# Kernel optimization log

Hardware: AMD Instinct MI355X
Metric: run time of the kernel (lower is better)

## Reference

```python
import math
import jax, jax.numpy as jnp
import numpy as np

EPS = 1e-5
B, S, D = 2, 2048, 2048
Z, HD, H, N = 512, 4096, 8, 8
ZH, VH = Z // H, HD // H  # 64, 512
GROUPS = 32


def timestep_norm(x, w, b):
    # cumulative (over time) group normalization; groups of dg channels
    dg = D // GROUPS
    xg = x.reshape(B, S, GROUPS, dg)
    s1 = jnp.cumsum(xg.sum(-1), axis=1)                 # [B,S,G]
    s2 = jnp.cumsum(jnp.square(xg).sum(-1), axis=1)     # [B,S,G]
    cnt = (jnp.arange(S, dtype=x.dtype) + 1.0) * dg
    mean = s1 / cnt[None, :, None]
    var = s2 / cnt[None, :, None] - jnp.square(mean)
    xn = (xg - mean[..., None]) * jax.lax.rsqrt(var[..., None] + EPS)
    return xn.reshape(B, S, D) * w + b


def cema(x, alpha, delta, theta, gamma, omega):
    # complex multi-head EMA: h_t = a*e^{i\theta} x_t + (1-a*d)*e^{i\theta} h_{t-1};
    # y_t = Re(gamma^H h_t) + omega * x_t    (real-arithmetic form, scan over time)
    p = jax.nn.sigmoid(alpha)                      # [D,N]
    qm = 1.0 - p * jax.nn.sigmoid(delta)           # [D,N]
    phase = jax.nn.sigmoid(theta)[:, None] * (2.0 * math.pi * (jnp.arange(N, dtype=x.dtype) + 1.0) / N)
    c, s = jnp.cos(phase), jnp.sin(phase)
    ur, ui = p * c, p * s
    qr, qi = qm * c, qm * s
    gr, gi = gamma[..., 0], gamma[..., 1]

    def step(h, xt):  # xt: [B,D]
        hr, hi = h
        nhr = qr * hr - qi * hi + ur * xt[..., None]
        nhi = qi * hr + qr * hi + ui * xt[..., None]
        y = jnp.sum(nhr * gr + nhi * gi, axis=-1)  # [B,D]
        return (nhr, nhi), y

    h0 = (jnp.zeros((B, D, N), x.dtype), jnp.zeros((B, D, N), x.dtype))
    _, ys = jax.lax.scan(step, h0, jnp.moveaxis(x, 1, 0))
    return jnp.moveaxis(ys, 0, 1) + x * omega


def rmsnorm(x, w=None):
    y = x * jax.lax.rsqrt(jnp.mean(jnp.square(x), axis=-1, keepdims=True) + EPS)
    return y if w is None else y * w


def apply_rotary(xq, xk, freqs):
    # xq/xk: [B,S,H,ZH]; freqs: [S, ZH//2, 2] (cos, sin)
    cos = freqs[None, :, None, :, 0]
    sin = freqs[None, :, None, :, 1]

    def rot(x):
        xr = x.reshape(*x.shape[:-1], ZH // 2, 2)
        re, im = xr[..., 0], xr[..., 1]
        out = jnp.stack([re * cos - im * sin, re * sin + im * cos], axis=-1)
        return out.reshape(x.shape)

    return rot(xq), rot(xk)


def setup_inputs():
    key = jax.random.key(0)
    ks = jax.random.split(key, 24)
    p = 0.02
    inp = {
        "x": jax.random.normal(ks[0], (B, S, D), jnp.float32),
        "tn_weight": 1.0 + p * jax.random.normal(ks[1], (D,), jnp.float32),
        "tn_bias": p * jax.random.normal(ks[2], (D,), jnp.float32),
        "ema_alpha": jax.random.normal(ks[3], (D, N), jnp.float32),
        "ema_delta": jax.random.normal(ks[4], (D, N), jnp.float32),
        "ema_theta": jax.random.normal(ks[5], (D,), jnp.float32),
        "ema_gamma": jax.random.normal(ks[6], (D, N, 2), jnp.float32) / math.sqrt(N),
        "ema_omega": p * jax.random.normal(ks[7], (D,), jnp.float32),
        "rms_weight": 1.0 + p * jax.random.normal(ks[8], (D,), jnp.float32),
        "wz_w": jax.random.normal(ks[9], (D, Z), jnp.float32) / math.sqrt(D),
        "wz_b": p * jax.random.normal(ks[10], (Z,), jnp.float32),
        "wv_w": jax.random.normal(ks[11], (D, HD), jnp.float32) / math.sqrt(D),
        "wv_b": p * jax.random.normal(ks[12], (HD,), jnp.float32),
        "wr_w": jax.random.normal(ks[13], (D, HD), jnp.float32) / math.sqrt(D),
        "wr_b": p * jax.random.normal(ks[14], (HD,), jnp.float32),
        "wh1_w": jax.random.normal(ks[15], (D, D), jnp.float32) / math.sqrt(D),
        "wh1_b": p * jax.random.normal(ks[16], (D,), jnp.float32),
        "wh2_w": jax.random.normal(ks[17], (HD, D), jnp.float32) / math.sqrt(HD),
        "attn_gamma": p * jax.random.normal(ks[18], (2, Z), jnp.float32),
        "attn_beta": p * jax.random.normal(ks[19], (2, Z), jnp.float32),
    }
    # rotary freqs (cos, sin) for head dim ZH
    inv = 1.0 / (10000.0 ** (np.arange(0, ZH, 2, dtype=np.float32) / ZH))
    ang = np.arange(S, dtype=np.float32)[:, None] * inv[None, :]
    inp["freqs_cis"] = jnp.asarray(np.stack([np.cos(ang), np.sin(ang)], axis=-1))
    return inp


def reference(x, freqs_cis, tn_weight, tn_bias, ema_alpha, ema_delta, ema_theta,
              ema_gamma, ema_omega, rms_weight, wz_w, wz_b, wv_w, wv_b, wr_w, wr_b,
              wh1_w, wh1_b, wh2_w, attn_gamma, attn_beta):
    residual = x
    out_tsn = timestep_norm(x, tn_weight, tn_bias)
    out_cema = cema(out_tsn, ema_alpha, ema_delta, ema_theta, ema_gamma, ema_omega)
    mx = rmsnorm(out_cema, rms_weight)

    z = mx @ wz_w + wz_b                              # [B,S,Z]
    z = rmsnorm(z.reshape(B, S, H, ZH)).reshape(B, S, Z)
    gamma = (attn_gamma + 1.0) / math.sqrt(ZH)        # [2,Z]
    z2 = z[:, :, None, :] * gamma + attn_beta         # [B,S,2,Z]
    q, k = z2[:, :, 0], z2[:, :, 1]

    v = jax.nn.silu(out_tsn @ wv_w + wv_b)            # [B,S,HD]
    r = jax.nn.silu(mx @ wr_w + wr_b)                 # [B,S,HD]

    qh = q.reshape(B, S, H, ZH)
    kh = k.reshape(B, S, H, ZH)
    vh = v.reshape(B, S, H, VH)
    qh, kh = apply_rotary(qh, kh, freqs_cis)

    # causal additive mask; scale 1.0 (folded into gamma)
    neg = jnp.finfo(jnp.float32).min
    mask = jnp.where(jnp.tril(jnp.ones((S, S), bool)), 0.0, neg).astype(jnp.float32)
    scores = jnp.einsum('bqhd,bkhd->bhqk', qh, kh) + mask
    probs = jax.nn.softmax(scores.astype(jnp.float32), axis=-1).astype(qh.dtype)
    attn = jnp.einsum('bhqk,bkhd->bqhd', probs, vh).reshape(B, S, HD)

    attn = attn * r
    h = (mx @ wh1_w + wh1_b) + attn @ wh2_w
    return h + residual
```

## Files before the change

### kernel.cpp

```cpp
#include <hip/hip_runtime.h>
#include <stdint.h>


typedef __bf16 bf16_t;
typedef bf16_t bf16x8 __attribute__((ext_vector_type(8)));
typedef float floatx4 __attribute__((ext_vector_type(4)));
typedef __attribute__((address_space(1))) unsigned int as1_uint;
typedef __attribute__((address_space(3))) unsigned int as3_uint;

static constexpr int kB = 2, kS = 2048, kD = 2048;
static constexpr int kZ = 512, kHD = 4096, kH = 8;
static constexpr int kG = 32;
static constexpr int kC = 64, kL = 32;

__device__ __forceinline__ void async16(void* lds, const void* g) {
  __builtin_amdgcn_global_load_lds((const as1_uint*)(size_t)g, (as3_uint*)lds, 16, 0, 0);
}

__device__ __forceinline__ float sigm(float x) { return 1.0f / (1.0f + expf(-x)); }

__global__ __launch_bounds__(256) void wtrans_all(
    const float* __restrict__ wz_w, const float* __restrict__ wv_w,
    const float* __restrict__ wr_w, const float* __restrict__ wh1_w,
    const float* __restrict__ wh2_w, bf16_t* __restrict__ wzT,
    bf16_t* __restrict__ wvT, bf16_t* __restrict__ wrT,
    bf16_t* __restrict__ whcT) {
  __shared__ float tile[32][33];
  const int bid = blockIdx.x;
  const float* W; bf16_t* Wt; int N, ldWt, colOff, nb, sub;
  if (bid < 1024)       { sub = bid;         W = wz_w;  Wt = wzT;  N = kZ;  ldWt = kD;   colOff = 0;    nb = 16;  }
  else if (bid < 9216)  { sub = bid - 1024;  W = wv_w;  Wt = wvT;  N = kHD; ldWt = kD;   colOff = 0;    nb = 128; }
  else if (bid < 17408) { sub = bid - 9216;  W = wr_w;  Wt = wrT;  N = kHD; ldWt = kD;   colOff = 0;    nb = 128; }
  else if (bid < 21504) { sub = bid - 17408; W = wh1_w; Wt = whcT; N = kD;  ldWt = 6144; colOff = 0;    nb = 64;  }
  else                  { sub = bid - 21504; W = wh2_w; Wt = whcT; N = kD;  ldWt = 6144; colOff = 2048; nb = 64;  }
  const int n0 = (sub % nb) * 32, k0 = (sub / nb) * 32;
  const int tx = threadIdx.x & 31, ty = threadIdx.x >> 5;
#pragma unroll
  for (int i = 0; i < 32; i += 8)
    tile[ty + i][tx] = W[(size_t)(k0 + ty + i) * N + n0 + tx];
  __syncthreads();
#pragma unroll
  for (int i = 0; i < 32; i += 8)
    Wt[(size_t)(n0 + ty + i) * ldWt + colOff + k0 + tx] = (bf16_t)tile[tx][ty + i];
}

__global__ __launch_bounds__(256) void tsn_sums(const float* __restrict__ x,
                                                float* __restrict__ g1,
                                                float* __restrict__ g2) {
  int bs = blockIdx.x, t = threadIdx.x;
  const float4* rp = (const float4*)(x + (size_t)bs * kD + t * 8);
  float4 a = rp[0], b = rp[1];
  float s1 = a.x + a.y + a.z + a.w + b.x + b.y + b.z + b.w;
  float s2 = a.x * a.x + a.y * a.y + a.z * a.z + a.w * a.w +
             b.x * b.x + b.y * b.y + b.z * b.z + b.w * b.w;
  s1 += __shfl_xor(s1, 1); s2 += __shfl_xor(s2, 1);
  s1 += __shfl_xor(s1, 2); s2 += __shfl_xor(s2, 2);
  s1 += __shfl_xor(s1, 4); s2 += __shfl_xor(s2, 4);
  if ((t & 7) == 0) {
    int g = t >> 3, b_ = bs >> 11, s = bs & 2047;
    size_t idx = ((size_t)b_ * kG + g) * kS + s;
    g1[idx] = s1; g2[idx] = s2;
  }
}

__global__ __launch_bounds__(256) void tsn_scan(float* __restrict__ g1,
                                                float* __restrict__ g2) {
  __shared__ float wt1[4], wt2[4];
  const int t = threadIdx.x, lane = t & 63, wv = t >> 6;
  size_t base = (size_t)blockIdx.x * kS + t * 8;
  float4 p0 = ((const float4*)(g1 + base))[0];
  float4 p1 = ((const float4*)(g1 + base))[1];
  float4 q0 = ((const float4*)(g2 + base))[0];
  float4 q1 = ((const float4*)(g2 + base))[1];
  float v1[8] = {p0.x, p0.y, p0.z, p0.w, p1.x, p1.y, p1.z, p1.w};
  float v2[8] = {q0.x, q0.y, q0.z, q0.w, q1.x, q1.y, q1.z, q1.w};
  float a1[8], a2[8], s1 = 0.f, s2 = 0.f;
#pragma unroll
  for (int i = 0; i < 8; ++i) {
    s1 += v1[i]; a1[i] = s1;
    s2 += v2[i]; a2[i] = s2;
  }
  float w1 = s1, w2 = s2;
#pragma unroll
  for (int off = 1; off < 64; off <<= 1) {
    float t1 = __shfl_up(w1, off), t2 = __shfl_up(w2, off);
    if (lane >= off) { w1 += t1; w2 += t2; }
  }
  if (lane == 63) { wt1[wv] = w1; wt2[wv] = w2; }
  __syncthreads();
  float add1 = w1 - s1, add2 = w2 - s2;
#pragma unroll
  for (int j = 0; j < 4; ++j)
    if (j < wv) { add1 += wt1[j]; add2 += wt2[j]; }
#pragma unroll
  for (int i = 0; i < 8; ++i) { a1[i] += add1; a2[i] += add2; }
  ((float4*)(g1 + base))[0] = make_float4(a1[0], a1[1], a1[2], a1[3]);
  ((float4*)(g1 + base))[1] = make_float4(a1[4], a1[5], a1[6], a1[7]);
  ((float4*)(g2 + base))[0] = make_float4(a2[0], a2[1], a2[2], a2[3]);
  ((float4*)(g2 + base))[1] = make_float4(a2[4], a2[5], a2[6], a2[7]);
}

__global__ __launch_bounds__(256) void tsn_norm(const float* __restrict__ x,
    const float* __restrict__ g1, const float* __restrict__ g2,
    const float* __restrict__ w, const float* __restrict__ bias,
    float* __restrict__ tsn, bf16_t* __restrict__ tsnb) {
  int bs = blockIdx.x, t = threadIdx.x;
  int b = bs >> 11, s = bs & 2047, g = t >> 3;
  float cnt = (float)(s + 1) * 64.0f;
  size_t gidx = ((size_t)b * kG + g) * kS + s;
  float mean = g1[gidx] / cnt;
  float inv = rsqrtf(g2[gidx] / cnt - mean * mean + 1e-5f);
  size_t base = (size_t)bs * kD + t * 8;
  float4 a = ((const float4*)(x + base))[0];
  float4 c = ((const float4*)(x + base))[1];
  float v[8] = {a.x, a.y, a.z, a.w, c.x, c.y, c.z, c.w};
  float4 w0 = ((const float4*)(w + t * 8))[0], w1 = ((const float4*)(w + t * 8))[1];
  float4 b0 = ((const float4*)(bias + t * 8))[0], b1 = ((const float4*)(bias + t * 8))[1];
  float wv[8] = {w0.x, w0.y, w0.z, w0.w, w1.x, w1.y, w1.z, w1.w};
  float bv[8] = {b0.x, b0.y, b0.z, b0.w, b1.x, b1.y, b1.z, b1.w};
  float r[8];
  bf16x8 ob;
#pragma unroll
  for (int i = 0; i < 8; ++i) {
    r[i] = (v[i] - mean) * inv * wv[i] + bv[i];
    ob[i] = (bf16_t)r[i];
  }
  ((float4*)(tsn + base))[0] = make_float4(r[0], r[1], r[2], r[3]);
  ((float4*)(tsn + base))[1] = make_float4(r[4], r[5], r[6], r[7]);
  *(bf16x8*)(tsnb + base) = ob;
}

__device__ __forceinline__ void cema_coeffs(const float* __restrict__ alpha,
    const float* __restrict__ delta, float st, int d,
    float (&qr)[8], float (&qi)[8], float (&ur)[8], float (&ui)[8]) {
  const float4* ap = (const float4*)(alpha + (size_t)d * 8);
  const float4* dp = (const float4*)(delta + (size_t)d * 8);
  float4 a0 = ap[0], a1 = ap[1], d0 = dp[0], d1 = dp[1];
  float av[8] = {a0.x, a0.y, a0.z, a0.w, a1.x, a1.y, a1.z, a1.w};
  float dv[8] = {d0.x, d0.y, d0.z, d0.w, d1.x, d1.y, d1.z, d1.w};
#pragma unroll
  for (int n = 0; n < 8; ++n) {
    float p = sigm(av[n]);
    float qm = 1.0f - p * sigm(dv[n]);
    float ph = st * (0.78539816339744831f * (float)(n + 1));
    float cs = cosf(ph), sn = sinf(ph);
    qr[n] = qm * cs; qi[n] = qm * sn;
    ur[n] = p * cs;  ui[n] = p * sn;
  }
}

__global__ __launch_bounds__(256) void cema_pass1(const float* __restrict__ tsn,
    const float* __restrict__ alpha, const float* __restrict__ delta,
    const float* __restrict__ theta, float2* __restrict__ hend) {
  int b = blockIdx.x >> 6, c = blockIdx.x & 63;
  int d = blockIdx.y * 256 + threadIdx.x;
  float st = sigm(theta[d]);
  float qr[8], qi[8], ur[8], ui[8];
  cema_coeffs(alpha, delta, st, d, qr, qi, ur, ui);
  float hr[8] = {0}, hi[8] = {0};
  const float* xp = tsn + ((size_t)b * kS + c * kL) * kD + d;
  for (int i = 0; i < kL; ++i) {
    float xt = xp[(size_t)i * kD];
#pragma unroll
    for (int n = 0; n < 8; ++n) {
      float tr = fmaf(qr[n], hr[n], fmaf(-qi[n], hi[n], ur[n] * xt));
      float ti = fmaf(qi[n], hr[n], fmaf(qr[n], hi[n], ui[n] * xt));
      hr[n] = tr; hi[n] = ti;
    }
  }
  float2* op = hend + (((size_t)(b * kC + c)) * kD + d) * 8;
#pragma unroll
  for (int n = 0; n < 8; ++n) op[n] = make_float2(hr[n], hi[n]);
}

__global__ __launch_bounds__(256) void cema_pass2(const float2* __restrict__ hend,
    const float* __restrict__ alpha, const float* __restrict__ delta,
    const float* __restrict__ theta, float2* __restrict__ hinit) {
  int tid = blockIdx.x * 256 + threadIdx.x;
  int n = tid & 7, d = (tid >> 3) & 2047, b = tid >> 14;
  int dn = d * 8 + n;
  float p = sigm(alpha[dn]);
  float qm = 1.0f - p * sigm(delta[dn]);
  float ph = sigm(theta[d]) * (0.78539816339744831f * (float)(n + 1));
  float ar = qm * cosf(ph), ai = qm * sinf(ph);
#pragma unroll
  for (int t = 0; t < 5; ++t) {
    float nr = ar * ar - ai * ai;
    ai = 2.0f * ar * ai;
    ar = nr;
  }
  float hr = 0.f, hi = 0.f;
  for (int c = 0; c < kC; ++c) {
    size_t idx = (((size_t)(b * kC + c)) * kD + d) * 8 + n;
    hinit[idx] = make_float2(hr, hi);
    float2 e = hend[idx];
    float nr = fmaf(ar, hr, fmaf(-ai, hi, e.x));
    float ni = fmaf(ai, hr, fmaf(ar, hi, e.y));
    hr = nr; hi = ni;
  }
}

__global__ __launch_bounds__(256) void cema_pass3(const float* __restrict__ tsn,
    const float* __restrict__ alpha, const float* __restrict__ delta,
    const float* __restrict__ theta, const float* __restrict__ gamma,
    const float* __restrict__ omega, const float2* __restrict__ hinit,
    float* __restrict__ outc) {
  int b = blockIdx.x >> 6, c = blockIdx.x & 63;
  int d = blockIdx.y * 256 + threadIdx.x;
  float st = sigm(theta[d]);
  float qr[8], qi[8], ur[8], ui[8];
  cema_coeffs(alpha, delta, st, d, qr, qi, ur, ui);
  float gr[8], gi[8];
  const float4* gp = (const float4*)(gamma + (size_t)d * 16);
#pragma unroll
  for (int m = 0; m < 4; ++m) {
    float4 g = gp[m];
    gr[m * 2] = g.x; gi[m * 2] = g.y; gr[m * 2 + 1] = g.z; gi[m * 2 + 1] = g.w;
  }
  float om = omega[d];
  float hr[8], hi[8];
  const float2* ip = hinit + (((size_t)(b * kC + c)) * kD + d) * 8;
#pragma unroll
  for (int n = 0; n < 8; ++n) { float2 h = ip[n]; hr[n] = h.x; hi[n] = h.y; }
  const float* xp = tsn + ((size_t)b * kS + c * kL) * kD + d;
  float* op = outc + ((size_t)b * kS + c * kL) * kD + d;
  for (int i = 0; i < kL; ++i) {
    float xt = xp[(size_t)i * kD];
    float y = 0.f;
#pragma unroll
    for (int n = 0; n < 8; ++n) {
      float tr = fmaf(qr[n], hr[n], fmaf(-qi[n], hi[n], ur[n] * xt));
      float ti = fmaf(qi[n], hr[n], fmaf(qr[n], hi[n], ui[n] * xt));
      hr[n] = tr; hi[n] = ti;
      y = fmaf(tr, gr[n], fmaf(ti, gi[n], y));
    }
    op[(size_t)i * kD] = fmaf(xt, om, y);
  }
}

__global__ __launch_bounds__(256) void rms_kernel(const float* __restrict__ in,
                                                  const float* __restrict__ w,
                                                  bf16_t* __restrict__ outb) {
  int bs = blockIdx.x, t = threadIdx.x;
  size_t base = (size_t)bs * kD + t * 8;
  float4 a = ((const float4*)(in + base))[0];
  float4 c = ((const float4*)(in + base))[1];
  float v[8] = {a.x, a.y, a.z, a.w, c.x, c.y, c.z, c.w};
  float ss = 0.f;
#pragma unroll
  for (int i = 0; i < 8; ++i) ss += v[i] * v[i];
#pragma unroll
  for (int off = 1; off < 64; off <<= 1) ss += __shfl_xor(ss, off);
  __shared__ float red[4];
  if ((t & 63) == 0) red[t >> 6] = ss;
  __syncthreads();
  ss = red[0] + red[1] + red[2] + red[3];
  float inv = rsqrtf(ss * (1.0f / 2048.0f) + 1e-5f);
  float4 w0 = ((const float4*)(w + t * 8))[0], w1 = ((const float4*)(w + t * 8))[1];
  float wv[8] = {w0.x, w0.y, w0.z, w0.w, w1.x, w1.y, w1.z, w1.w};
  bf16x8 ob;
#pragma unroll
  for (int i = 0; i < 8; ++i) ob[i] = (bf16_t)(v[i] * inv * wv[i]);
  *(bf16x8*)(outb + base) = ob;
}

__global__ __launch_bounds__(256) void zpost_kernel(const float* __restrict__ z,
    const float* __restrict__ ag, const float* __restrict__ ab,
    const float* __restrict__ freqs, bf16_t* __restrict__ q, bf16_t* __restrict__ k) {
  int bs = blockIdx.x, t = threadIdx.x;
  int b = bs >> 11, s = bs & 2047;
  int h = t >> 5, i = t & 31;
  const float* zr = z + (size_t)bs * kZ + h * 64;
  float re = zr[2 * i], im = zr[2 * i + 1];
  float ss = re * re + im * im;
#pragma unroll
  for (int off = 1; off < 32; off <<= 1) ss += __shfl_xor(ss, off);
  float inv = rsqrtf(ss * (1.0f / 64.0f) + 1e-5f);
  float zne = re * inv, zno = im * inv;
  const float rs = 0.125f;
  int ze = h * 64 + 2 * i, zo = ze + 1;
  float qe = zne * ((ag[ze] + 1.f) * rs) + ab[ze];
  float qo = zno * ((ag[zo] + 1.f) * rs) + ab[zo];
  float ke = zne * ((ag[kZ + ze] + 1.f) * rs) + ab[kZ + ze];
  float ko = zno * ((ag[kZ + zo] + 1.f) * rs) + ab[kZ + zo];
  float cs = freqs[((size_t)s * 32 + i) * 2 + 0];
  float sn = freqs[((size_t)s * 32 + i) * 2 + 1];
  size_t o = (((size_t)b * kH + h) * kS + s) * 64 + 2 * i;
  q[o]     = (bf16_t)(qe * cs - qo * sn);
  q[o + 1] = (bf16_t)(qe * sn + qo * cs);
  k[o]     = (bf16_t)(ke * cs - ko * sn);
  k[o + 1] = (bf16_t)(ke * sn + ko * cs);
}

__global__ __launch_bounds__(256) void gemm_fused3(
    const bf16_t* __restrict__ tsnb, const bf16_t* __restrict__ mx,
    const bf16_t* __restrict__ wvT, const bf16_t* __restrict__ wrT,
    const bf16_t* __restrict__ wzT, const float* __restrict__ wv_b,
    const float* __restrict__ wr_b, const float* __restrict__ wz_b,
    bf16_t* __restrict__ vTb, bf16_t* __restrict__ rb,
    float* __restrict__ zbuf) {
  __shared__ __align__(16) bf16_t sA[2][128 * 32];
  __shared__ __align__(16) bf16_t sB[2][128 * 32];
  const int bid = blockIdx.x;
  const bf16_t* A; const bf16_t* Bt; const float* bias;
  int N, epi, sub;
  if (bid < 1024)      { sub = bid;        A = tsnb; Bt = wvT; bias = wv_b; N = kHD; epi = 1; }
  else if (bid < 2048) { sub = bid - 1024; A = mx;   Bt = wrT; bias = wr_b; N = kHD; epi = 2; }
  else                 { sub = bid - 2048; A = mx;   Bt = wzT; bias = wz_b; N = kZ;  epi = 0; }
  const int m0 = (sub & 31) * 128, n0 = (sub >> 5) * 128;
  const int t = threadIdx.x;
  const int wave = t >> 6, lane = t & 63;
  const int quad = lane >> 4, l16 = lane & 15;
  const int wm = (wave >> 1) * 64, wn = (wave & 1) * 64;
  const int K = kD;

  floatx4 acc[4][4];
#pragma unroll
  for (int i = 0; i < 4; ++i)
#pragma unroll
    for (int j = 0; j < 4; ++j) acc[i][j] = (floatx4){0.f, 0.f, 0.f, 0.f};

  const int seg0 = wave * 64 + lane;
  const int seg1 = 256 + wave * 64 + lane;
  const int r0 = seg0 >> 2, c0 = (seg0 & 3) * 8;
  const int r1 = seg1 >> 2, c1 = (seg1 & 3) * 8;

  auto stage = [&](int buf, int kt) {
    async16(sA[buf] + (size_t)(wave * 64) * 8,       A + (size_t)(m0 + r0) * K + kt + c0);
    async16(sA[buf] + (size_t)(256 + wave * 64) * 8, A + (size_t)(m0 + r1) * K + kt + c1);
    async16(sB[buf] + (size_t)(wave * 64) * 8,       Bt + (size_t)(n0 + r0) * K + kt + c0);
    async16(sB[buf] + (size_t)(256 + wave * 64) * 8, Bt + (size_t)(n0 + r1) * K + kt + c1);
  };

  stage(0, 0);
  __syncthreads();

  const int nsteps = K >> 5;
  for (int st = 0; st < nsteps; ++st) {
    const int cur = st & 1;
    if (st + 1 < nsteps) stage(cur ^ 1, (st + 1) << 5);

    bf16x8 af[4], bfr[4];
#pragma unroll
    for (int i = 0; i < 4; ++i)
      af[i] = *(const bf16x8*)(sA[cur] + (wm + i * 16 + l16) * 32 + quad * 8);
#pragma unroll
    for (int j = 0; j < 4; ++j)
      bfr[j] = *(const bf16x8*)(sB[cur] + (wn + j * 16 + l16) * 32 + quad * 8);
#pragma unroll
    for (int i = 0; i < 4; ++i)
#pragma unroll
      for (int j = 0; j < 4; ++j)
        acc[i][j] = __builtin_amdgcn_mfma_f32_16x16x32_bf16(af[i], bfr[j], acc[i][j], 0, 0, 0);

    __syncthreads();
  }

#pragma unroll
  for (int i = 0; i < 4; ++i) {
#pragma unroll
    for (int j = 0; j < 4; ++j) {
#pragma unroll
      for (int r = 0; r < 4; ++r) {
        int row = m0 + wm + i * 16 + quad * 4 + r;
        int col = n0 + wn + j * 16 + l16;
        size_t idx = (size_t)row * N + col;
        float v = acc[i][j][r];
        if (epi == 0) {
          zbuf[idx] = v + bias[col];
        } else if (epi == 1) {
          v += bias[col];
          v = v / (1.f + __expf(-v));
          size_t vidx = ((size_t)(row >> 11) * kHD + col) * (size_t)kS + (row & 2047);
          vTb[vidx] = (bf16_t)v;
        } else {
          v += bias[col];
          v = v / (1.f + __expf(-v));
          rb[idx] = (bf16_t)v;
        }
      }
    }
  }
}

__global__ __launch_bounds__(256) void gemm_bt(const bf16_t* __restrict__ A1,
    int lda1, const bf16_t* __restrict__ A2, int lda2, int K1,
    const bf16_t* __restrict__ Bt, int M, int N, int K,
    const float* __restrict__ bias, const float* __restrict__ add1,
    float* __restrict__ outF) {
  __shared__ __align__(16) bf16_t sA[2][128 * 32];
  __shared__ __align__(16) bf16_t sB[2][128 * 32];
  const int t = threadIdx.x;
  const int wave = t >> 6, lane = t & 63;
  const int quad = lane >> 4, l16 = lane & 15;
  const int m0 = blockIdx.x * 128, n0 = blockIdx.y * 128;
  const int wm = (wave >> 1) * 64, wn = (wave & 1) * 64;

  floatx4 acc[4][4];
#pragma unroll
  for (int i = 0; i < 4; ++i)
#pragma unroll
    for (int j = 0; j < 4; ++j) acc[i][j] = (floatx4){0.f, 0.f, 0.f, 0.f};

  const int seg0 = wave * 64 + lane;
  const int seg1 = 256 + wave * 64 + lane;
  const int r0 = seg0 >> 2, c0 = (seg0 & 3) * 8;
  const int r1 = seg1 >> 2, c1 = (seg1 & 3) * 8;

  auto stage = [&](int buf, int kt) {
    const bf16_t* Ab; int ldab; int kk;
    if (kt < K1) { Ab = A1; ldab = lda1; kk = kt; }
    else         { Ab = A2; ldab = lda2; kk = kt - K1; }
    async16(sA[buf] + (size_t)(wave * 64) * 8,       Ab + (size_t)(m0 + r0) * ldab + kk + c0);
    async16(sA[buf] + (size_t)(256 + wave * 64) * 8, Ab + (size_t)(m0 + r1) * ldab + kk + c1);
    async16(sB[buf] + (size_t)(wave * 64) * 8,       Bt + (size_t)(n0 + r0) * K + kt + c0);
    async16(sB[buf] + (size_t)(256 + wave * 64) * 8, Bt + (size_t)(n0 + r1) * K + kt + c1);
  };

  stage(0, 0);
  __syncthreads();

  const int nsteps = K >> 5;
  for (int st = 0; st < nsteps; ++st) {
    const int cur = st & 1;
    if (st + 1 < nsteps) stage(cur ^ 1, (st + 1) << 5);

    bf16x8 af[4], bfr[4];
#pragma unroll
    for (int i = 0; i < 4; ++i)
      af[i] = *(const bf16x8*)(sA[cur] + (wm + i * 16 + l16) * 32 + quad * 8);
#pragma unroll
    for (int j = 0; j < 4; ++j)
      bfr[j] = *(const bf16x8*)(sB[cur] + (wn + j * 16 + l16) * 32 + quad * 8);
#pragma unroll
    for (int i = 0; i < 4; ++i)
#pragma unroll
      for (int j = 0; j < 4; ++j)
        acc[i][j] = __builtin_amdgcn_mfma_f32_16x16x32_bf16(af[i], bfr[j], acc[i][j], 0, 0, 0);

    __syncthreads();
  }

#pragma unroll
  for (int i = 0; i < 4; ++i) {
#pragma unroll
    for (int j = 0; j < 4; ++j) {
#pragma unroll
      for (int r = 0; r < 4; ++r) {
        int row = m0 + wm + i * 16 + quad * 4 + r;
        int col = n0 + wn + j * 16 + l16;
        size_t idx = (size_t)row * N + col;
        outF[idx] = acc[i][j][r] + bias[col] + add1[idx];
      }
    }
  }
}

__global__ __launch_bounds__(256) void attn_kernel(const bf16_t* __restrict__ qg,
    const bf16_t* __restrict__ kg, const bf16_t* __restrict__ vT,
    const bf16_t* __restrict__ rg, bf16_t* __restrict__ attnG) {
  const int bid = blockIdx.x;
  const int qt = (kS / 64 - 1) - (bid >> 5);
  const int bh = (bid >> 1) & 15;
  const int vs = bid & 1;
  const int b = bh >> 3, h = bh & 7;
  const int t = threadIdx.x;
  const int w = t >> 6, lane = t & 63;
  const int quad = lane >> 4, l16 = lane & 15;
  const int q0 = qt * 64;

  __shared__ __align__(16) bf16_t sP[2][64 * 64];
  __shared__ __align__(16) bf16_t sK[2][64 * 64];
  __shared__ float sM[64], sL[64], sAl[2][64];
  if (t < 64) { sM[t] = 0.f; sL[t] = 0.f; }

  const bf16_t* qbase = qg + ((size_t)bh * kS + q0) * 64;
  const bf16_t* kbase = kg + (size_t)bh * kS * 64;
  const bf16_t* vbase = vT + ((size_t)bh * 512 + vs * 256 + w * 64) * kS;

  auto stage_k = [&](bf16_t* dstbuf, int k0) {
#pragma unroll
    for (int half = 0; half < 2; ++half) {
      int seg = half * 256 + w * 64 + lane;
      int r = seg >> 3, cc = seg & 7;
      async16(dstbuf + (size_t)(half * 256 + w * 64) * 8,
              kbase + (size_t)(k0 + r) * 64 + (cc ^ (r & 7)) * 8);
    }
  };

  bf16x8 qfrag[2];
#pragma unroll
  for (int ks = 0; ks < 2; ++ks)
    qfrag[ks] = *(const bf16x8*)(qbase + (size_t)(w * 16 + l16) * 64 + ks * 32 + quad * 8);

  floatx4 oacc[4][4];
#pragma unroll
  for (int i = 0; i < 4; ++i)
#pragma unroll
    for (int j = 0; j < 4; ++j) oacc[i][j] = (floatx4){0.f, 0.f, 0.f, 0.f};

  stage_k(sK[0], 0);
  __syncthreads();

  for (int kt = 0; kt <= qt; ++kt) {
    const int k0 = kt * 64;
    const int pb = kt & 1;

    if (kt < qt) stage_k(sK[pb ^ 1], k0 + 64);

    bf16x8 vf[2][4];
#pragma unroll
    for (int ks = 0; ks < 2; ++ks)
#pragma unroll
      for (int nj = 0; nj < 4; ++nj)
        vf[ks][nj] = *(const bf16x8*)(vbase + (size_t)(nj * 16 + l16) * kS + k0 + ks * 32 + quad * 8);

    floatx4 sacc[4];
#pragma unroll
    for (int nt = 0; nt < 4; ++nt) sacc[nt] = (floatx4){0.f, 0.f, 0.f, 0.f};
#pragma unroll
    for (int ks = 0; ks < 2; ++ks)
#pragma unroll
      for (int nt = 0; nt < 4; ++nt) {
        int row = nt * 16 + l16;
        int ch = (ks * 4 + quad) ^ (row & 7);
        bf16x8 kf = *(const bf16x8*)(sK[pb] + row * 64 + ch * 8);
        sacc[nt] = __builtin_amdgcn_mfma_f32_16x16x32_bf16(qfrag[ks], kf, sacc[nt], 0, 0, 0);
      }
    if (kt == qt) {
#pragma unroll
      for (int nt = 0; nt < 4; ++nt)
#pragma unroll
        for (int r = 0; r < 4; ++r) {
          int sk = k0 + nt * 16 + l16;
          int qq = q0 + w * 16 + quad * 4 + r;
          if (sk > qq) sacc[nt][r] = -1e30f;
        }
    }

    float mo[4], mloc[4], lspec[4];
#pragma unroll
    for (int r = 0; r < 4; ++r) {
      mo[r] = sM[w * 16 + quad * 4 + r];
      mloc[r] = fmaxf(fmaxf(sacc[0][r], sacc[1][r]), fmaxf(sacc[2][r], sacc[3][r]));
    }
#pragma unroll
    for (int r = 0; r < 4; ++r) {
      float s = 0.f;
#pragma unroll
      for (int nt = 0; nt < 4; ++nt) {
        float e = __expf(sacc[nt][r] - mo[r]);
        sacc[nt][r] = e;
        s += e;
      }
      lspec[r] = s;
    }
#pragma unroll
    for (int off = 1; off < 16; off <<= 1)
#pragma unroll
      for (int r = 0; r < 4; ++r) {
        mloc[r] = fmaxf(mloc[r], __shfl_xor(mloc[r], off));
        lspec[r] += __shfl_xor(lspec[r], off);
      }
    float mnew[4], al[4];
#pragma unroll
    for (int r = 0; r < 4; ++r) {
      mnew[r] = fmaxf(mo[r], mloc[r]);
      al[r] = __expf(mo[r] - mnew[r]);
    }
    if (l16 == 0) {
#pragma unroll
      for (int r = 0; r < 4; ++r) {
        int row = w * 16 + quad * 4 + r;
        sM[row] = mnew[r];
        sL[row] = al[r] * (sL[row] + lspec[r]);
        sAl[pb][row] = al[r];
      }
    }
#pragma unroll
    for (int nt = 0; nt < 4; ++nt)
#pragma unroll
      for (int r = 0; r < 4; ++r) {
        int row = w * 16 + quad * 4 + r;
        sP[pb][row * 64 + ((nt * 16 + l16) ^ ((row & 7) << 3))] = (bf16_t)(sacc[nt][r] * al[r]);
      }

    __syncthreads();

#pragma unroll
    for (int mi = 0; mi < 4; ++mi)
#pragma unroll
      for (int r = 0; r < 4; ++r) {
        float a = sAl[pb][mi * 16 + quad * 4 + r];
#pragma unroll
        for (int nj = 0; nj < 4; ++nj) oacc[mi][nj][r] *= a;
      }
    __builtin_amdgcn_s_setprio(1);
#pragma unroll
    for (int ks = 0; ks < 2; ++ks) {
      bf16x8 pa[4];
#pragma unroll
      for (int mi = 0; mi < 4; ++mi) {
        int row = mi * 16 + l16;
        pa[mi] = *(const bf16x8*)(sP[pb] + row * 64 + ((ks * 32 + quad * 8) ^ ((row & 7) << 3)));
      }
#pragma unroll
      for (int nj = 0; nj < 4; ++nj)
#pragma unroll
        for (int mi = 0; mi < 4; ++mi)
          oacc[mi][nj] = __builtin_amdgcn_mfma_f32_16x16x32_bf16(pa[mi], vf[ks][nj], oacc[mi][nj], 0, 0, 0);
    }
    __builtin_amdgcn_s_setprio(0);
  }

#pragma unroll
  for (int mi = 0; mi < 4; ++mi)
#pragma unroll
    for (int r = 0; r < 4; ++r) {
      int srow = q0 + mi * 16 + quad * 4 + r;
      float linv = 1.0f / sL[mi * 16 + quad * 4 + r];
#pragma unroll
      for (int nj = 0; nj < 4; ++nj) {
        int hd = h * 512 + vs * 256 + w * 64 + nj * 16 + l16;
        size_t idx = ((size_t)b * kS + srow) * kHD + hd;
        float rv = (float)rg[idx];
        attnG[idx] = (bf16_t)(oacc[mi][nj][r] * linv * rv);
      }
    }
}

extern "C" void kernel_launch(void* const* d_in, const int* in_sizes, int n_in,
                              void* d_out, int out_size, void* d_ws, size_t ws_size,
                              hipStream_t stream) {
  const float* x      = (const float*)d_in[0];
  const float* tnw    = (const float*)d_in[1];
  const float* tnb    = (const float*)d_in[2];
  const float* ealpha = (const float*)d_in[3];
  const float* edelta = (const float*)d_in[4];
  const float* etheta = (const float*)d_in[5];
  const float* egamma = (const float*)d_in[6];
  const float* eomega = (const float*)d_in[7];
  const float* rmsw   = (const float*)d_in[8];
  const float* wz_w   = (const float*)d_in[9];
  const float* wz_b   = (const float*)d_in[10];
  const float* wv_w   = (const float*)d_in[11];
  const float* wv_b   = (const float*)d_in[12];
  const float* wr_w   = (const float*)d_in[13];
  const float* wr_b   = (const float*)d_in[14];
  const float* wh1_w  = (const float*)d_in[15];
  const float* wh1_b  = (const float*)d_in[16];
  const float* wh2_w  = (const float*)d_in[17];
  const float* ag     = (const float*)d_in[18];
  const float* ab     = (const float*)d_in[19];
  const float* freqs  = (const float*)d_in[20];
  float* out = (float*)d_out;

  char* ws = (char*)d_ws;
  size_t off = 0;
  auto alloc = [&](size_t bytes) -> void* {
    void* p = ws + off;
    off += (bytes + 255) & ~(size_t)255;
    return p;
  };
  float*  tsn  = (float*)alloc(8388608ull * 4);
  bf16_t* tsnb = (bf16_t*)alloc(8388608ull * 2);
  float*  g1   = (float*)alloc(131072ull * 4);
  float*  g2   = (float*)alloc(131072ull * 4);
  float*  cema = (float*)alloc(8388608ull * 4);
  bf16_t* mx   = (bf16_t*)alloc(8388608ull * 2);
  bf16_t* wzT  = (bf16_t*)alloc(1048576ull * 2);
  bf16_t* wvT  = (bf16_t*)alloc(8388608ull * 2);
  bf16_t* wrT  = (bf16_t*)alloc(8388608ull * 2);
  bf16_t* whcT = (bf16_t*)alloc(12582912ull * 2);
  float*  zbuf = (float*)alloc(2097152ull * 4);
  bf16_t* qb   = (bf16_t*)alloc(2097152ull * 2);
  bf16_t* kb   = (bf16_t*)alloc(2097152ull * 2);
  bf16_t* rb   = (bf16_t*)alloc(16777216ull * 2);
  bf16_t* aG   = (bf16_t*)alloc(16777216ull * 2);
  bf16_t* vTb  = (bf16_t*)tsn;
  float*  h1   = cema;
  float2* hend  = (float2*)rb;
  float2* hinit = (float2*)aG;
  (void)h1;

  wtrans_all<<<dim3(29696), 256, 0, stream>>>(wz_w, wv_w, wr_w, wh1_w, wh2_w,
                                              wzT, wvT, wrT, whcT);

  tsn_sums<<<kB * kS, 256, 0, stream>>>(x, g1, g2);
  tsn_scan<<<kB * kG, 256, 0, stream>>>(g1, g2);
  tsn_norm<<<kB * kS, 256, 0, stream>>>(x, g1, g2, tnw, tnb, tsn, tsnb);

  cema_pass1<<<dim3(kB * kC, kD / 256), 256, 0, stream>>>(tsn, ealpha, edelta,
                                                          etheta, hend);
  cema_pass2<<<kB * kD * 8 / 256, 256, 0, stream>>>(hend, ealpha, edelta,
                                                    etheta, hinit);
  cema_pass3<<<dim3(kB * kC, kD / 256), 256, 0, stream>>>(tsn, ealpha, edelta,
      etheta, egamma, eomega, hinit, cema);
  rms_kernel<<<kB * kS, 256, 0, stream>>>(cema, rmsw, mx);

  const int M = kB * kS;
  gemm_fused3<<<dim3(2176), 256, 0, stream>>>(tsnb, mx, wvT, wrT, wzT,
      wv_b, wr_b, wz_b, vTb, rb, zbuf);
  zpost_kernel<<<kB * kS, 256, 0, stream>>>(zbuf, ag, ab, freqs, qb, kb);
  attn_kernel<<<dim3(1024), 256, 0, stream>>>(qb, kb, vTb, rb, aG);
  gemm_bt<<<dim3(M / 128, kD / 128), 256, 0, stream>>>(mx, kD, aG, kHD, kD,
      whcT, M, kD, 6144, wh1_b, x, out);
  (void)in_sizes; (void)n_in; (void)out_size; (void)ws_size;
}
```

Baseline: 835.8 us.

## Use 8-wave blocks for final GEMM and XCD-aware attention block mapping

The final output GEMM now runs with 512 threads (8 waves) per 128x128 tile, each wave computing a 64x32 sub-tile, so each thread issues half as many async loads and holds half the accumulators. This aims to raise occupancy and latency hiding for the K=6144 GEMM. The attention kernel's block-index decode is also remapped so that each (batch, head) is pinned to one XCD (bid&7), meant to improve L2 reuse of K/V across query tiles. Risks: smaller per-wave tiles lower MFMA-to-LDS-read ratio and add sync cost.

```diff
diff --git a/kernel.cpp b/kernel.cpp
--- a/kernel.cpp
+++ b/kernel.cpp
@@ -383,38 +383,33 @@
   }
 }
 
-__global__ __launch_bounds__(256) void gemm_bt(const bf16_t* __restrict__ A1,
-    int lda1, const bf16_t* __restrict__ A2, int lda2, int K1,
-    const bf16_t* __restrict__ Bt, int M, int N, int K,
-    const float* __restrict__ bias, const float* __restrict__ add1,
+__global__ __launch_bounds__(512) void gemm_whc8(const bf16_t* __restrict__ mx,
+    const bf16_t* __restrict__ aG, const bf16_t* __restrict__ whcT,
+    const float* __restrict__ wh1_b, const float* __restrict__ x,
     float* __restrict__ outF) {
   __shared__ __align__(16) bf16_t sA[2][128 * 32];
   __shared__ __align__(16) bf16_t sB[2][128 * 32];
   const int t = threadIdx.x;
-  const int wave = t >> 6, lane = t & 63;
+  const int wid = t >> 6, lane = t & 63;
   const int quad = lane >> 4, l16 = lane & 15;
   const int m0 = blockIdx.x * 128, n0 = blockIdx.y * 128;
-  const int wm = (wave >> 1) * 64, wn = (wave & 1) * 64;
-
-  floatx4 acc[4][4];
+  const int wm = (wid >> 2) * 64, wn = (wid & 3) * 32;
+  const int N = kD, K = 6144, K1 = kD;
+
+  floatx4 acc[4][2];
 #pragma unroll
   for (int i = 0; i < 4; ++i)
 #pragma unroll
-    for (int j = 0; j < 4; ++j) acc[i][j] = (floatx4){0.f, 0.f, 0.f, 0.f};
-
-  const int seg0 = wave * 64 + lane;
-  const int seg1 = 256 + wave * 64 + lane;
-  const int r0 = seg0 >> 2, c0 = (seg0 & 3) * 8;
-  const int r1 = seg1 >> 2, c1 = (seg1 & 3) * 8;
+    for (int j = 0; j < 2; ++j) acc[i][j] = (floatx4){0.f, 0.f, 0.f, 0.f};
+
+  const int r0 = t >> 2, c0 = (t & 3) * 8;
 
   auto stage = [&](int buf, int kt) {
     const bf16_t* Ab; int ldab; int kk;
-    if (kt < K1) { Ab = A1; ldab = lda1; kk = kt; }
-    else         { Ab = A2; ldab = lda2; kk = kt - K1; }
-    async16(sA[buf] + (size_t)(wave * 64) * 8,       Ab + (size_t)(m0 + r0) * ldab + kk + c0);
-    async16(sA[buf] + (size_t)(256 + wave * 64) * 8, Ab + (size_t)(m0 + r1) * ldab + kk + c1);
-    async16(sB[buf] + (size_t)(wave * 64) * 8,       Bt + (size_t)(n0 + r0) * K + kt + c0);
-    async16(sB[buf] + (size_t)(256 + wave * 64) * 8, Bt + (size_t)(n0 + r1) * K + kt + c1);
+    if (kt < K1) { Ab = mx; ldab = kD;  kk = kt; }
+    else         { Ab = aG; ldab = kHD; kk = kt - K1; }
+    async16(sA[buf] + (size_t)(wid * 64) * 8, Ab + (size_t)(m0 + r0) * ldab + kk + c0);
+    async16(sB[buf] + (size_t)(wid * 64) * 8, whcT + (size_t)(n0 + r0) * 6144 + kt + c0);
   };
 
   stage(0, 0);
@@ -425,44 +420,43 @@
     const int cur = st & 1;
     if (st + 1 < nsteps) stage(cur ^ 1, (st + 1) << 5);
 
-    bf16x8 af[4], bfr[4];
+    bf16x8 af[4], bfr[2];
 #pragma unroll
     for (int i = 0; i < 4; ++i)
       af[i] = *(const bf16x8*)(sA[cur] + (wm + i * 16 + l16) * 32 + quad * 8);
 #pragma unroll
-    for (int j = 0; j < 4; ++j)
+    for (int j = 0; j < 2; ++j)
       bfr[j] = *(const bf16x8*)(sB[cur] + (wn + j * 16 + l16) * 32 + quad * 8);
 #pragma unroll
     for (int i = 0; i < 4; ++i)
 #pragma unroll
-      for (int j = 0; j < 4; ++j)
+      for (int j = 0; j < 2; ++j)
         acc[i][j] = __builtin_amdgcn_mfma_f32_16x16x32_bf16(af[i], bfr[j], acc[i][j], 0, 0, 0);
 
     __syncthreads();
   }
 
 #pragma unroll
-  for (int i = 0; i < 4; ++i) {
-#pragma unroll
-    for (int j = 0; j < 4; ++j) {
+  for (int i = 0; i < 4; ++i)
+#pragma unroll
+    for (int j = 0; j < 2; ++j)
 #pragma unroll
       for (int r = 0; r < 4; ++r) {
         int row = m0 + wm + i * 16 + quad * 4 + r;
         int col = n0 + wn + j * 16 + l16;
         size_t idx = (size_t)row * N + col;
-        outF[idx] = acc[i][j][r] + bias[col] + add1[idx];
-      }
-    }
-  }
+        outF[idx] = acc[i][j][r] + wh1_b[col] + x[idx];
+      }
 }
 
 __global__ __launch_bounds__(256) void attn_kernel(const bf16_t* __restrict__ qg,
     const bf16_t* __restrict__ kg, const bf16_t* __restrict__ vT,
     const bf16_t* __restrict__ rg, bf16_t* __restrict__ attnG) {
   const int bid = blockIdx.x;
-  const int qt = (kS / 64 - 1) - (bid >> 5);
-  const int bh = (bid >> 1) & 15;
-  const int vs = bid & 1;
+  const int xcd = bid & 7, kk = bid >> 3;
+  const int qt = (kS / 64 - 1) - (kk >> 2);
+  const int bh = (((kk >> 1) & 1) << 3) | xcd;
+  const int vs = kk & 1;
   const int b = bh >> 3, h = bh & 7;
   const int t = threadIdx.x;
   const int w = t >> 6, lane = t & 63;
@@ -678,10 +672,8 @@
   bf16_t* rb   = (bf16_t*)alloc(16777216ull * 2);
   bf16_t* aG   = (bf16_t*)alloc(16777216ull * 2);
   bf16_t* vTb  = (bf16_t*)tsn;
-  float*  h1   = cema;
   float2* hend  = (float2*)rb;
   float2* hinit = (float2*)aG;
-  (void)h1;
 
   wtrans_all<<<dim3(29696), 256, 0, stream>>>(wz_w, wv_w, wr_w, wh1_w, wh2_w,
                                               wzT, wvT, wrT, whcT);
@@ -703,7 +695,7 @@
       wv_b, wr_b, wz_b, vTb, rb, zbuf);
   zpost_kernel<<<kB * kS, 256, 0, stream>>>(zbuf, ag, ab, freqs, qb, kb);
   attn_kernel<<<dim3(1024), 256, 0, stream>>>(qb, kb, vTb, rb, aG);
-  gemm_bt<<<dim3(M / 128, kD / 128), 256, 0, stream>>>(mx, kD, aG, kHD, kD,
-      whcT, M, kD, 6144, wh1_b, x, out);
+  gemm_whc8<<<dim3(M / 128, kD / 128), 512, 0, stream>>>(mx, aG, whcT,
+      wh1_b, x, out);
   (void)in_sizes; (void)n_in; (void)out_size; (void)ws_size;
 }
```

New measurement: 840.1 us. No clear change (+0.5%).
